# Performance work log

Measured on AMD Instinct MI355X. Metric: run time of the kernel, lower is better.

The kernel has to match this reference:

```python
import jax, jax.numpy as jnp
import numpy as np

K = 50          # NEC paper uses p=50 neighbors
DELTA = 1e-3    # kernel smoothing constant


def setup_inputs() -> dict:
    key = jax.random.key(0)
    ks = jax.random.split(key, 8)
    B, D_IN, D, A, C = 512, 2, 128, 3, 200000
    s = lambda fan_in: 1.0 / np.sqrt(fan_in)
    return {
        "x": jax.random.normal(ks[0], (B, D_IN), jnp.float32),
        "W1": jax.random.normal(ks[1], (D_IN, D), jnp.float32) * s(D_IN),
        "b1": jnp.zeros((D,), jnp.float32),
        "W2": jax.random.normal(ks[2], (D, D), jnp.float32) * s(D),
        "b2": jnp.zeros((D,), jnp.float32),
        "W3": jax.random.normal(ks[3], (D, D), jnp.float32) * s(D),
        "b3": jnp.zeros((D,), jnp.float32),
        "W4": jax.random.normal(ks[4], (D, D), jnp.float32) * s(D),
        "b4": jnp.zeros((D,), jnp.float32),
        "keys": jax.random.normal(ks[5], (A, C, D), jnp.float32),
        "mem_values": jax.random.normal(ks[6], (A, C), jnp.float32),
    }


def _encode(x, W1, b1, W2, b2, W3, b3, W4, b4):
    h = jax.nn.relu(x @ W1 + b1)
    h = jax.nn.relu(h @ W2 + b2)
    h = jax.nn.relu(h @ W3 + b3)
    return h @ W4 + b4  # [B, D]


def _dnd_lookup(h, keys, mem_values):
    # h: [B, D]; keys: [A, C, D]; mem_values: [A, C]
    q2 = jnp.sum(h * h, axis=-1)                       # [B]
    k2 = jnp.sum(keys * keys, axis=-1)                 # [A, C]
    cross = jnp.einsum("bd,acd->bac", h, keys)         # [B, A, C]
    d2 = jnp.maximum(q2[:, None, None] + k2[None] - 2.0 * cross, 0.0)
    neg_d, idx = jax.lax.top_k(-d2, K)                  # [B, A, K]
    d_top = -neg_d
    w = 1.0 / (d_top + DELTA)                           # NEC kernel
    w = w / jnp.sum(w, axis=-1, keepdims=True)
    a_idx = jnp.arange(keys.shape[0])[None, :, None]    # [1, A, 1]
    v_top = mem_values[a_idx, idx]                      # gather -> [B, A, K]
    values = jnp.sum(w * v_top, axis=-1)                # [B, A]
    return values


def reference(x, W1, b1, W2, b2, W3, b3, W4, b4, keys, mem_values):
    h = _encode(x, W1, b1, W2, b2, W3, b3, W4, b4)
    values = _dnd_lookup(h, keys, mem_values)
    actions = jnp.argmax(values, axis=-1)
    return values, actions
```

## Files before the change

kernel.cpp:

```cpp
#include <hip/hip_runtime.h>
#include <hip/hip_bf16.h>
#include <math.h>

#define B_    512
#define DIM   128
#define A_    3
#define C_    200000
#define K_    50
#define DELTA 1e-3

typedef __attribute__((ext_vector_type(8))) short bf16x8;
typedef __attribute__((ext_vector_type(4))) float f32x4;

#define NBIN_A 128
#define CAP_A  1024
#define ROWCH  12500

#define NSEG3  128
#define TPS3   25
#define NT3    3125

#define AOFF_H64   0u
#define AOFF_H32   524288u
#define AOFF_HBF   786432u
#define AOFF_Q2    917504u
#define AOFF_V64   1718272u
#define AOFF_BINS  8022016u
#define NEED_A     (8022016ull + 307200000ull)

#define NBIN_B 192
#define CAP_B  768
#define BM_B   64
#define BN_B   128
#define TPC_B  16
#define CHUNK_B (TPC_B*BN_B)
#define NCH_B  ((C_ + CHUNK_B - 1)/CHUNK_B)

#define BOFF_H32   0u
#define BOFF_H64   262144u
#define BOFF_Q2    786432u
#define BOFF_K2    788480u
#define BOFF_HIST  3188480u
#define BOFF_TAU   4368128u
#define BOFF_CNT   4374272u
#define BOFF_V64   4380416u
#define BOFF_CAND  4392704u

static __device__ inline unsigned short f2bf(float x) {
    union { float f; unsigned u; } c; c.f = x;
    unsigned r = (c.u + 0x7FFFu + ((c.u >> 16) & 1u)) >> 16;
    return (unsigned short)r;
}
static __device__ inline unsigned pkbf(float a, float b) {
    __hip_bfloat162 t = __float22bfloat162_rn(make_float2(a, b));
    union { __hip_bfloat162 h; unsigned u; } cv; cv.h = t; return cv.u;
}

__global__ __launch_bounds__(128) void mlp_kernel(
    const float* __restrict__ x,
    const float* __restrict__ W1, const float* __restrict__ b1,
    const float* __restrict__ W2, const float* __restrict__ b2,
    const float* __restrict__ W3, const float* __restrict__ b3,
    const float* __restrict__ W4, const float* __restrict__ b4,
    float* __restrict__ h32, unsigned short* __restrict__ hbf,
    double* __restrict__ h64, float* __restrict__ q2)
{
    int b = blockIdx.x, t = threadIdx.x;
    __shared__ double s0[DIM], s1[DIM];
    double x0 = (double)x[b*2+0], x1 = (double)x[b*2+1];
    double h = x0*(double)W1[t] + x1*(double)W1[DIM+t] + (double)b1[t];
    s0[t] = h > 0.0 ? h : 0.0;
    __syncthreads();
    double acc = (double)b2[t];
    for (int k = 0; k < DIM; k++) acc += s0[k]*(double)W2[k*DIM+t];
    s1[t] = acc > 0.0 ? acc : 0.0;
    __syncthreads();
    acc = (double)b3[t];
    for (int k = 0; k < DIM; k++) acc += s1[k]*(double)W3[k*DIM+t];
    s0[t] = acc > 0.0 ? acc : 0.0;
    __syncthreads();
    acc = (double)b4[t];
    for (int k = 0; k < DIM; k++) acc += s0[k]*(double)W4[k*DIM+t];
    h64[b*DIM+t] = acc;
    float hf = (float)acc;
    h32[b*DIM+t] = hf;
    hbf[b*DIM+t] = f2bf(hf);
    s1[t] = acc*acc;
    __syncthreads();
    for (int s = 64; s > 0; s >>= 1) { if (t < s) s1[t] += s1[t+s]; __syncthreads(); }
    if (t == 0) q2[b] = (float)s1[0];
}

static __device__ inline void load4(float4 lv[4], const float* __restrict__ ka,
                                    int nrow, int hh) {
    const float4* gp = (const float4*)(ka + (size_t)nrow*DIM) + hh*4;
    #pragma unroll
    for (int qq = 0; qq < 4; qq++) lv[qq] = gp[qq];
}
static __device__ inline void conv_store(const float4 lv[4], char* sBn,
                                         float* k2n, int r, int hh) {
    float ss = 0.f;
    int4 pk0, pk1;
    {
        float4 v0 = lv[0], v1 = lv[1];
        ss += v0.x*v0.x + v0.y*v0.y + v0.z*v0.z + v0.w*v0.w
            + v1.x*v1.x + v1.y*v1.y + v1.z*v1.z + v1.w*v1.w;
        pk0.x = (int)pkbf(v0.x, v0.y); pk0.y = (int)pkbf(v0.z, v0.w);
        pk0.z = (int)pkbf(v1.x, v1.y); pk0.w = (int)pkbf(v1.z, v1.w);
    }
    {
        float4 v0 = lv[2], v1 = lv[3];
        ss += v0.x*v0.x + v0.y*v0.y + v0.z*v0.z + v0.w*v0.w
            + v1.x*v1.x + v1.y*v1.y + v1.z*v1.z + v1.w*v1.w;
        pk1.x = (int)pkbf(v0.x, v0.y); pk1.y = (int)pkbf(v0.z, v0.w);
        pk1.z = (int)pkbf(v1.x, v1.y); pk1.w = (int)pkbf(v1.z, v1.w);
    }
    char* base = sBn + r*256;
    *(int4*)(base + (((hh*2    ) ^ (r & 7)) << 4)) = pk0;
    *(int4*)(base + (((hh*2 + 1) ^ (r & 7)) << 4)) = pk1;
    ss += __shfl_xor(ss, 1, 64);
    ss += __shfl_xor(ss, 2, 64);
    ss += __shfl_xor(ss, 4, 64);
    if (hh == 0) k2n[r] = ss;
}

__global__ __launch_bounds__(512, 2) void gemm3_kernel(
    const float* __restrict__ keys, const unsigned short* __restrict__ hbf,
    const float* __restrict__ q2, unsigned char* __restrict__ bins)
{
    const int seg = blockIdx.x, my = blockIdx.y, a = blockIdx.z;
    const int b0 = my*128;
    const int tid = threadIdx.x;
    const int lane = tid & 63, w = tid >> 6;
    const int lm = lane & 15, kh = lane >> 4;
    const int wn = w & 1, wm = w >> 1;

    const int tbeg = seg*TPS3;
    int tcnt = NT3 - tbeg;
    if (tcnt <= 0) return;
    if (tcnt > TPS3) tcnt = TPS3;

    __shared__ __align__(16) short sA[16384];
    __shared__ __align__(16) short sB[2][8192];
    __shared__ float q2s[128];
    __shared__ float k2s[2][64];

    {
        int r4 = tid >> 2, h4 = tid & 3;
        const int4* gp = (const int4*)hbf + (size_t)(b0 + r4)*16 + h4*4;
        #pragma unroll
        for (int qq = 0; qq < 4; qq++) {
            int cc = h4*4 + qq;
            *(int4*)((char*)sA + r4*256 + ((cc ^ (r4 & 7)) << 4)) = gp[qq];
        }
        if (tid < 128) q2s[tid] = q2[b0 + tid];
    }

    const int r = tid >> 3, hh = tid & 7;
    const float* ka = keys + (size_t)a*C_*DIM;

    float4 lv[4];
    load4(lv, ka, tbeg*64 + r, hh);
    conv_store(lv, (char*)&sB[0][0], k2s[0], r, hh);
    __syncthreads();

    int cur = 0;
    for (int t = 0; t < tcnt; t++) {
        const int n0 = (tbeg + t)*64;
        const bool more = (t + 1 < tcnt);

        if (more) load4(lv, ka, n0 + 64 + r, hh);

        f32x4 acc[2][2];
        #pragma unroll
        for (int i = 0; i < 2; i++)
            #pragma unroll
            for (int j = 0; j < 2; j++) acc[i][j] = (f32x4){0.f, 0.f, 0.f, 0.f};

        const char* sBc = (const char*)&sB[cur][0];
        #pragma unroll
        for (int kst = 0; kst < 4; kst++) {
            bf16x8 af[2], bfv[2];
            #pragma unroll
            for (int i = 0; i < 2; i++) {
                int nr = wn*32 + i*16 + lm;
                af[i] = *(const bf16x8*)(sBc + nr*256 + ((((kst<<2) + kh) ^ (nr & 7)) << 4));
            }
            #pragma unroll
            for (int j = 0; j < 2; j++) {
                int br = wm*32 + j*16 + lm;
                bfv[j] = *(const bf16x8*)((const char*)sA + br*256 + ((((kst<<2) + kh) ^ (br & 7)) << 4));
            }
            #pragma unroll
            for (int i = 0; i < 2; i++)
                #pragma unroll
                for (int j = 0; j < 2; j++)
                    acc[i][j] = __builtin_amdgcn_mfma_f32_16x16x32_bf16(af[i], bfv[j], acc[i][j], 0, 0, 0);
        }

        unsigned char* bp = bins + ((size_t)(a*B_ + b0))*C_ + n0;
        #pragma unroll
        for (int i = 0; i < 2; i++) {
            int nl = wn*32 + i*16 + kh*4;
            float4 kq = *(const float4*)&k2s[cur][nl];
            #pragma unroll
            for (int j = 0; j < 2; j++) {
                int bcol = wm*32 + j*16 + lm;
                float q2v = q2s[bcol];
                unsigned pk = 0;
                #pragma unroll
                for (int rg = 0; rg < 4; rg++) {
                    float kv = (rg == 0) ? kq.x : (rg == 1) ? kq.y : (rg == 2) ? kq.z : kq.w;
                    float d2v = (q2v + kv) - 2.0f*acc[i][j][rg];
                    float dc = fminf(fmaxf(d2v, 16.0f), 4095.0f);
                    unsigned bin = (__float_as_uint(dc) >> 19) - 2096u;
                    pk |= bin << (8*rg);
                }
                *(unsigned*)(bp + (size_t)bcol*C_ + nl) = pk;
            }
        }

        if (more) conv_store(lv, (char*)&sB[cur ^ 1][0], k2s[cur ^ 1], r, hh);
        __syncthreads();
        cur ^= 1;
    }
}

__global__ __launch_bounds__(256) void finish_kernel(
    const unsigned char* __restrict__ bins, const float* __restrict__ keys,
    const double* __restrict__ h64, const float* __restrict__ mem_values,
    float* __restrict__ out_values, double* __restrict__ val64)
{
    const int q = blockIdx.x;
    const int a = q >> 9, b = q & 511;
    const int p = b*A_ + a;
    const int tid = threadIdx.x;

    __shared__ unsigned hist_s[NBIN_A*8];
    __shared__ unsigned hc[NBIN_A];
    __shared__ double hd[DIM];
    __shared__ int    cidx[CAP_A];
    __shared__ double d2s[CAP_A];
    __shared__ float  vs[CAP_A];
    __shared__ double redv[4];
    __shared__ int    redi4[4];
    __shared__ double acc_w, acc_wv;
    __shared__ unsigned cnt_s;
    __shared__ int thr_s;

    for (int i = tid; i < NBIN_A*8; i += 256) hist_s[i] = 0;
    for (int i = tid; i < DIM; i += 256) hd[i] = h64[(size_t)b*DIM + i];
    if (tid == 0) { cnt_s = 0; acc_w = 0.0; acc_wv = 0.0; }
    __syncthreads();

    const uint4* row = (const uint4*)(bins + (size_t)q*C_);
    const int rep = tid & 7;
    for (int ch = tid; ch < ROWCH; ch += 256) {
        uint4 v = row[ch];
        unsigned d[4] = {v.x, v.y, v.z, v.w};
        #pragma unroll
        for (int e = 0; e < 4; e++) {
            unsigned x = d[e];
            atomicAdd(&hist_s[((x      ) & 127u)*8 + rep], 1u);
            atomicAdd(&hist_s[((x >>  8) & 127u)*8 + rep], 1u);
            atomicAdd(&hist_s[((x >> 16) & 127u)*8 + rep], 1u);
            atomicAdd(&hist_s[((x >> 24) & 127u)*8 + rep], 1u);
        }
    }
    __syncthreads();
    if (tid < NBIN_A) {
        unsigned s = 0;
        #pragma unroll
        for (int r2 = 0; r2 < 8; r2++) s += hist_s[tid*8 + r2];
        hc[tid] = s;
    }
    __syncthreads();
    if (tid == 0) {
        unsigned cum = 0; int jsel = NBIN_A-1;
        for (int j = 0; j < NBIN_A; j++) { cum += hc[j]; if (cum >= K_) { jsel = j; break; } }
        unsigned c1 = cum + (jsel+1 < NBIN_A ? hc[jsel+1] : 0u);
        unsigned c2 = c1  + (jsel+2 < NBIN_A ? hc[jsel+2] : 0u);
        int jt = (c2 <= 768u) ? jsel+2 : jsel+1;
        if (jt > NBIN_A-1) jt = NBIN_A-1;
        thr_s = jt + 1;
    }
    __syncthreads();
    const unsigned thr  = (unsigned)thr_s;
    const unsigned addv = (128u - thr) * 0x01010101u;
    for (int ch = tid; ch < ROWCH; ch += 256) {
        uint4 v = row[ch];
        unsigned d[4] = {v.x, v.y, v.z, v.w};
        #pragma unroll
        for (int e = 0; e < 4; e++) {
            unsigned m = (d[e] + addv) & 0x80808080u;
            if (m != 0x80808080u) {
                #pragma unroll
                for (int by = 0; by < 4; by++) {
                    if (!((m >> (8*by + 7)) & 1u)) {
                        unsigned pos = atomicAdd(&cnt_s, 1u);
                        if (pos < CAP_A) cidx[pos] = ch*16 + e*4 + by;
                    }
                }
            }
        }
    }
    __syncthreads();
    int n = (int)cnt_s; if (n > CAP_A) n = CAP_A;

    for (int i = tid; i < n; i += 256) {
        int c = cidx[i];
        const float4* kr = (const float4*)(keys + ((size_t)a*C_ + c)*DIM);
        double s0 = 0.0, s1 = 0.0;
        #pragma unroll 4
        for (int kq = 0; kq < 32; kq++) {
            float4 kv = kr[kq];
            double d0 = hd[4*kq+0] - (double)kv.x;
            double d1 = hd[4*kq+1] - (double)kv.y;
            double d2 = hd[4*kq+2] - (double)kv.z;
            double d3 = hd[4*kq+3] - (double)kv.w;
            s0 += d0*d0 + d1*d1; s1 += d2*d2 + d3*d3;
        }
        d2s[i] = s0 + s1;
        vs[i]  = mem_values[(size_t)a*C_ + c];
    }
    __syncthreads();

    int kk = n < K_ ? n : K_;
    for (int t = 0; t < kk; t++) {
        double best = 1e300; int bi = -1;
        for (int i = tid; i < n; i += 256)
            if (d2s[i] < best) { best = d2s[i]; bi = i; }
        #pragma unroll
        for (int off = 32; off > 0; off >>= 1) {
            double ov = __shfl_xor(best, off, 64);
            int    oi = __shfl_xor(bi,   off, 64);
            if (ov < best) { best = ov; bi = oi; }
        }
        int wv = tid >> 6;
        if ((tid & 63) == 0) { redv[wv] = best; redi4[wv] = bi; }
        __syncthreads();
        if (tid == 0) {
            double bv = redv[0]; int wi = redi4[0];
            if (redv[1] < bv) { bv = redv[1]; wi = redi4[1]; }
            if (redv[2] < bv) { bv = redv[2]; wi = redi4[2]; }
            if (redv[3] < bv) { bv = redv[3]; wi = redi4[3]; }
            double d = d2s[wi]; if (d < 0.0) d = 0.0;
            double wgt = 1.0 / (d + DELTA);
            acc_w += wgt; acc_wv += wgt * (double)vs[wi];
            d2s[wi] = 2e300;
        }
        __syncthreads();
    }
    if (tid == 0) {
        double v = acc_wv / acc_w;
        out_values[p] = (float)v;
        val64[p] = v;
    }
}

__global__ __launch_bounds__(256) void k2_kernel(const float* __restrict__ keys,
                                                 float* __restrict__ k2)
{
    int r = blockIdx.x*4 + (threadIdx.x >> 6);
    int lane = threadIdx.x & 63;
    float2 v = ((const float2*)keys)[(size_t)r*64 + lane];
    float s = v.x*v.x + v.y*v.y;
    #pragma unroll
    for (int off = 32; off > 0; off >>= 1) s += __shfl_down(s, off, 64);
    if (lane == 0) k2[r] = s;
}

template<int MODE>
__global__ __launch_bounds__(256) void pass_kernel(
    const float* __restrict__ keys, const float* __restrict__ h32,
    const float* __restrict__ q2,   const float* __restrict__ k2,
    unsigned* __restrict__ hist,    const float* __restrict__ tau,
    unsigned* __restrict__ cnt,     int* __restrict__ cand)
{
    const int bt = blockIdx.x;
    const int ch = blockIdx.y;
    const int a  = blockIdx.z;
    const int b0 = bt*BM_B;
    const int tid = threadIdx.x;
    const int tx = tid & 31, ty = tid >> 5;

    __shared__ float4 hs4[BM_B*33];
    __shared__ float4 ks4[BN_B*33];
    __shared__ float  q2s[BM_B];
    __shared__ float  taus[BM_B];
    __shared__ unsigned hist_s[MODE == 0 ? BM_B*NBIN_B : 1];

    #pragma unroll
    for (int q = 0; q < BM_B*32/256; q++) {
        int flat = q*256 + tid; int row = flat >> 5, kq = flat & 31;
        hs4[row*33 + kq] = ((const float4*)h32)[(size_t)(b0+row)*32 + kq];
    }
    if (tid < BM_B) {
        q2s[tid] = q2[b0+tid];
        if (MODE == 1) taus[tid] = tau[(b0+tid)*A_ + a];
    }
    if (MODE == 0) for (int i = tid; i < BM_B*NBIN_B; i += 256) hist_s[i] = 0;
    const float* __restrict__ k2g = k2 + (size_t)a*C_;

    for (int t = 0; t < TPC_B; t++) {
        int n0 = ch*CHUNK_B + t*BN_B;
        if (n0 >= C_) break;
        __syncthreads();
        #pragma unroll
        for (int q = 0; q < 16; q++) {
            int flat = q*256 + tid; int row = flat >> 5, kq = flat & 31;
            int nr = n0 + row; if (nr >= C_) nr = C_-1;
            ks4[row*33 + kq] = ((const float4*)keys)[((size_t)a*C_ + nr)*32 + kq];
        }
        __syncthreads();

        float acc[8][4];
        #pragma unroll
        for (int i = 0; i < 8; i++)
            #pragma unroll
            for (int j = 0; j < 4; j++) acc[i][j] = 0.0f;

        for (int kq = 0; kq < 32; kq++) {
            float4 hv[8], kv[4];
            #pragma unroll
            for (int i = 0; i < 8; i++) hv[i] = hs4[(ty*8+i)*33 + kq];
            #pragma unroll
            for (int j = 0; j < 4; j++) kv[j] = ks4[(j*32+tx)*33 + kq];
            #pragma unroll
            for (int i = 0; i < 8; i++)
                #pragma unroll
                for (int j = 0; j < 4; j++)
                    acc[i][j] += hv[i].x*kv[j].x + hv[i].y*kv[j].y
                               + hv[i].z*kv[j].z + hv[i].w*kv[j].w;
        }

        #pragma unroll
        for (int i = 0; i < 8; i++) {
            int bl = ty*8 + i;
            float q2b = q2s[bl];
            #pragma unroll
            for (int j = 0; j < 4; j++) {
                int n = n0 + j*32 + tx;
                if (n < C_) {
                    float d2f = fmaxf(q2b + k2g[n] - 2.0f*acc[i][j], 0.0f);
                    if (MODE == 0) {
                        int bin = (int)(__float_as_uint(d2f + 1.0f) >> 19) - 2032;
                        bin = bin < 0 ? 0 : (bin > NBIN_B-1 ? NBIN_B-1 : bin);
                        atomicAdd(&hist_s[bl*NBIN_B + bin], 1u);
                    } else {
                        if (d2f < taus[bl]) {
                            int p = (b0+bl)*A_ + a;
                            unsigned pos = atomicAdd(&cnt[p], 1u);
                            if (pos < CAP_B) cand[(size_t)p*CAP_B + pos] = n;
                        }
                    }
                }
            }
        }
    }
    if (MODE == 0) {
        __syncthreads();
        for (int i = tid; i < BM_B*NBIN_B; i += 256) {
            unsigned v = hist_s[i];
            if (v) {
                int bl = i / NBIN_B, bin = i % NBIN_B;
                atomicAdd(&hist[(size_t)((b0+bl)*A_ + a)*NBIN_B + bin], v);
            }
        }
    }
}

__global__ __launch_bounds__(256) void tauB_kernel(const unsigned* __restrict__ hist,
                                                   float* __restrict__ tau)
{
    int p = blockIdx.x*256 + threadIdx.x;
    if (p >= B_*A_) return;
    const unsigned* hp = hist + (size_t)p*NBIN_B;
    unsigned cum = 0; int jsel = NBIN_B-1;
    for (int j = 0; j < NBIN_B; j++) { cum += hp[j]; if (cum >= K_) { jsel = j; break; } }
    tau[p] = __uint_as_float((unsigned)(2034 + jsel) << 19) - 1.0f;
}

__global__ __launch_bounds__(256) void select_kernel(
    const float* __restrict__ keys, const double* __restrict__ h64,
    const float* __restrict__ mem_values,
    const unsigned* __restrict__ cnt, const int* __restrict__ cand,
    float* __restrict__ out_values, double* __restrict__ val64, int cap)
{
    int p = blockIdx.x; int b = p / A_, a = p % A_;
    int tid = threadIdx.x;
    __shared__ double hd[DIM];
    __shared__ double d2s[CAP_A];
    __shared__ float  vs[CAP_A];
    __shared__ double redv[4];
    __shared__ int    redi4[4];
    __shared__ double acc_w, acc_wv;

    for (int i = tid; i < DIM; i += 256) hd[i] = h64[(size_t)b*DIM + i];
    if (tid == 0) { acc_w = 0.0; acc_wv = 0.0; }
    __syncthreads();

    int n = (int)cnt[p]; if (n > cap) n = cap;
    for (int i = tid; i < n; i += 256) {
        int c = cand[(size_t)p*cap + i];
        const float4* kr = (const float4*)(keys + ((size_t)a*C_ + c)*DIM);
        double s0 = 0.0, s1 = 0.0;
        #pragma unroll 4
        for (int kq = 0; kq < 32; kq++) {
            float4 kv = kr[kq];
            double d0 = hd[4*kq+0] - (double)kv.x;
            double d1 = hd[4*kq+1] - (double)kv.y;
            double d2 = hd[4*kq+2] - (double)kv.z;
            double d3 = hd[4*kq+3] - (double)kv.w;
            s0 += d0*d0 + d1*d1; s1 += d2*d2 + d3*d3;
        }
        d2s[i] = s0 + s1;
        vs[i]  = mem_values[(size_t)a*C_ + c];
    }
    __syncthreads();

    int kk = n < K_ ? n : K_;
    for (int t = 0; t < kk; t++) {
        double best = 1e300; int bi = -1;
        for (int i = tid; i < n; i += 256)
            if (d2s[i] < best) { best = d2s[i]; bi = i; }
        #pragma unroll
        for (int off = 32; off > 0; off >>= 1) {
            double ov = __shfl_xor(best, off, 64);
            int    oi = __shfl_xor(bi,   off, 64);
            if (ov < best) { best = ov; bi = oi; }
        }
        int wv = tid >> 6;
        if ((tid & 63) == 0) { redv[wv] = best; redi4[wv] = bi; }
        __syncthreads();
        if (tid == 0) {
            double bv = redv[0]; int wi = redi4[0];
            if (redv[1] < bv) { bv = redv[1]; wi = redi4[1]; }
            if (redv[2] < bv) { bv = redv[2]; wi = redi4[2]; }
            if (redv[3] < bv) { bv = redv[3]; wi = redi4[3]; }
            double d = d2s[wi]; if (d < 0.0) d = 0.0;
            double wgt = 1.0 / (d + DELTA);
            acc_w += wgt; acc_wv += wgt * (double)vs[wi];
            d2s[wi] = 2e300;
        }
        __syncthreads();
    }
    if (tid == 0) {
        double v = acc_wv / acc_w;
        out_values[p] = (float)v;
        val64[p] = v;
    }
}

__global__ void argmax_kernel(const double* __restrict__ val64, float* __restrict__ out)
{
    int b = blockIdx.x*blockDim.x + threadIdx.x;
    if (b >= B_) return;
    double v0 = val64[b*A_+0], v1 = val64[b*A_+1], v2 = val64[b*A_+2];
    int bi = 0; double bv = v0;
    if (v1 > bv) { bv = v1; bi = 1; }
    if (v2 > bv) { bv = v2; bi = 2; }
    out[B_*A_ + b] = (float)bi;
}

extern "C" void kernel_launch(void* const* d_in, const int* in_sizes, int n_in,
                              void* d_out, int out_size, void* d_ws, size_t ws_size,
                              hipStream_t stream)
{
    const float* x    = (const float*)d_in[0];
    const float* W1   = (const float*)d_in[1];
    const float* b1   = (const float*)d_in[2];
    const float* W2   = (const float*)d_in[3];
    const float* b2   = (const float*)d_in[4];
    const float* W3   = (const float*)d_in[5];
    const float* b3   = (const float*)d_in[6];
    const float* W4   = (const float*)d_in[7];
    const float* b4   = (const float*)d_in[8];
    const float* keys = (const float*)d_in[9];
    const float* memv = (const float*)d_in[10];

    char* ws = (char*)d_ws;

    if (ws_size >= NEED_A) {
        double*         h64  = (double*)        (ws + AOFF_H64);
        float*          h32  = (float*)         (ws + AOFF_H32);
        unsigned short* hbf  = (unsigned short*)(ws + AOFF_HBF);
        float*          q2   = (float*)         (ws + AOFF_Q2);
        double*         v64  = (double*)        (ws + AOFF_V64);
        unsigned char*  bins = (unsigned char*) (ws + AOFF_BINS);

        mlp_kernel<<<B_, 128, 0, stream>>>(x, W1, b1, W2, b2, W3, b3, W4, b4, h32, hbf, h64, q2);
        gemm3_kernel<<<dim3(NSEG3, 4, A_), 512, 0, stream>>>(keys, hbf, q2, bins);
        finish_kernel<<<B_*A_, 256, 0, stream>>>(bins, keys, h64, memv, (float*)d_out, v64);
        argmax_kernel<<<2, 256, 0, stream>>>(v64, (float*)d_out);
    } else {
        float*          h32  = (float*)         (ws + BOFF_H32);
        double*         h64  = (double*)        (ws + BOFF_H64);
        float*          q2   = (float*)         (ws + BOFF_Q2);
        float*          k2   = (float*)         (ws + BOFF_K2);
        unsigned*       hist = (unsigned*)      (ws + BOFF_HIST);
        float*          tau  = (float*)         (ws + BOFF_TAU);
        unsigned*       cnt  = (unsigned*)      (ws + BOFF_CNT);
        double*         v64  = (double*)        (ws + BOFF_V64);
        int*            cand = (int*)           (ws + BOFF_CAND);
        unsigned short* hbf  = (unsigned short*)(ws + BOFF_CAND);

        hipMemsetAsync(ws + BOFF_HIST, 0, (BOFF_CNT + B_*A_*4) - BOFF_HIST, stream);

        mlp_kernel<<<B_, 128, 0, stream>>>(x, W1, b1, W2, b2, W3, b3, W4, b4, h32, hbf, h64, q2);
        k2_kernel<<<(A_*C_)/4, 256, 0, stream>>>(keys, k2);
        pass_kernel<0><<<dim3(B_/BM_B, NCH_B, A_), 256, 0, stream>>>(keys, h32, q2, k2, hist, nullptr, nullptr, nullptr);
        tauB_kernel<<<(B_*A_ + 255)/256, 256, 0, stream>>>(hist, tau);
        pass_kernel<1><<<dim3(B_/BM_B, NCH_B, A_), 256, 0, stream>>>(keys, h32, q2, k2, nullptr, tau, cnt, cand);
        select_kernel<<<B_*A_, 256, 0, stream>>>(keys, h64, memv, cnt, cand, (float*)d_out, v64, CAP_B);
        argmax_kernel<<<2, 256, 0, stream>>>(v64, (float*)d_out);
    }
}
```

Before: 960.1 us.

## Shrink GEMM query tile to 64 rows, defer bin stores, widen histogram replicas

The distance GEMM now processes 64 query rows per block instead of 128, with twice as many blocks and a launch bound of 6 blocks per SM. This lowers per-block LDS and register use so more blocks can be resident at once. Each tile's packed bin bytes are written one iteration later, so the global store overlaps the next tile's MFMA work. The finish kernel's shared histogram now keeps 16 replicas per bin, indexed by wave and lane, to reduce atomic contention. The cost is that each block re-reads the keys tile twice as often, which adds global traffic.

```diff
diff --git a/kernel.cpp b/kernel.cpp
--- a/kernel.cpp
+++ b/kernel.cpp
@@ -124,12 +124,12 @@
     if (hh == 0) k2n[r] = ss;
 }
 
-__global__ __launch_bounds__(512, 2) void gemm3_kernel(
+__global__ __launch_bounds__(512, 6) void gemm3_kernel(
     const float* __restrict__ keys, const unsigned short* __restrict__ hbf,
     const float* __restrict__ q2, unsigned char* __restrict__ bins)
 {
     const int seg = blockIdx.x, my = blockIdx.y, a = blockIdx.z;
-    const int b0 = my*128;
+    const int b0 = my*64;
     const int tid = threadIdx.x;
     const int lane = tid & 63, w = tid >> 6;
     const int lm = lane & 15, kh = lane >> 4;
@@ -140,20 +140,20 @@
     if (tcnt <= 0) return;
     if (tcnt > TPS3) tcnt = TPS3;
 
-    __shared__ __align__(16) short sA[16384];
+    __shared__ __align__(16) short sA[8192];
     __shared__ __align__(16) short sB[2][8192];
-    __shared__ float q2s[128];
+    __shared__ float q2s[64];
     __shared__ float k2s[2][64];
 
     {
-        int r4 = tid >> 2, h4 = tid & 3;
-        const int4* gp = (const int4*)hbf + (size_t)(b0 + r4)*16 + h4*4;
-        #pragma unroll
-        for (int qq = 0; qq < 4; qq++) {
-            int cc = h4*4 + qq;
-            *(int4*)((char*)sA + r4*256 + ((cc ^ (r4 & 7)) << 4)) = gp[qq];
-        }
-        if (tid < 128) q2s[tid] = q2[b0 + tid];
+        #pragma unroll
+        for (int u = 0; u < 2; u++) {
+            int idx = tid*2 + u;
+            int rr = idx >> 4, cc = idx & 15;
+            const int4 gv = ((const int4*)hbf)[(size_t)(b0 + rr)*16 + cc];
+            *(int4*)((char*)sA + rr*256 + ((cc ^ (rr & 7)) << 4)) = gv;
+        }
+        if (tid < 64) q2s[tid] = q2[b0 + tid];
     }
 
     const int r = tid >> 3, hh = tid & 7;
@@ -163,6 +163,14 @@
     load4(lv, ka, tbeg*64 + r, hh);
     conv_store(lv, (char*)&sB[0][0], k2s[0], r, hh);
     __syncthreads();
+
+    unsigned char* bp_base = bins + ((size_t)(a*B_ + b0))*C_;
+    const int bcol = wm*16 + lm;
+    const size_t soff0 = (size_t)bcol*C_ + (wn*32 + 0*16 + kh*4);
+    const size_t soff1 = (size_t)bcol*C_ + (wn*32 + 1*16 + kh*4);
+
+    unsigned pk_prev0 = 0, pk_prev1 = 0;
+    int n0_prev = 0;
 
     int cur = 0;
     for (int t = 0; t < tcnt; t++) {
@@ -170,60 +178,59 @@
         const bool more = (t + 1 < tcnt);
 
         if (more) load4(lv, ka, n0 + 64 + r, hh);
-
-        f32x4 acc[2][2];
-        #pragma unroll
-        for (int i = 0; i < 2; i++)
-            #pragma unroll
-            for (int j = 0; j < 2; j++) acc[i][j] = (f32x4){0.f, 0.f, 0.f, 0.f};
+        if (t > 0) {
+            *(unsigned*)(bp_base + n0_prev + soff0) = pk_prev0;
+            *(unsigned*)(bp_base + n0_prev + soff1) = pk_prev1;
+        }
+
+        f32x4 acc[2];
+        acc[0] = (f32x4){0.f, 0.f, 0.f, 0.f};
+        acc[1] = (f32x4){0.f, 0.f, 0.f, 0.f};
 
         const char* sBc = (const char*)&sB[cur][0];
         #pragma unroll
         for (int kst = 0; kst < 4; kst++) {
-            bf16x8 af[2], bfv[2];
+            bf16x8 af[2], bfv;
             #pragma unroll
             for (int i = 0; i < 2; i++) {
                 int nr = wn*32 + i*16 + lm;
                 af[i] = *(const bf16x8*)(sBc + nr*256 + ((((kst<<2) + kh) ^ (nr & 7)) << 4));
             }
-            #pragma unroll
-            for (int j = 0; j < 2; j++) {
-                int br = wm*32 + j*16 + lm;
-                bfv[j] = *(const bf16x8*)((const char*)sA + br*256 + ((((kst<<2) + kh) ^ (br & 7)) << 4));
+            {
+                int br = wm*16 + lm;
+                bfv = *(const bf16x8*)((const char*)sA + br*256 + ((((kst<<2) + kh) ^ (br & 7)) << 4));
             }
             #pragma unroll
             for (int i = 0; i < 2; i++)
-                #pragma unroll
-                for (int j = 0; j < 2; j++)
-                    acc[i][j] = __builtin_amdgcn_mfma_f32_16x16x32_bf16(af[i], bfv[j], acc[i][j], 0, 0, 0);
-        }
-
-        unsigned char* bp = bins + ((size_t)(a*B_ + b0))*C_ + n0;
-        #pragma unroll
-        for (int i = 0; i < 2; i++) {
-            int nl = wn*32 + i*16 + kh*4;
-            float4 kq = *(const float4*)&k2s[cur][nl];
-            #pragma unroll
-            for (int j = 0; j < 2; j++) {
-                int bcol = wm*32 + j*16 + lm;
-                float q2v = q2s[bcol];
+                acc[i] = __builtin_amdgcn_mfma_f32_16x16x32_bf16(af[i], bfv, acc[i], 0, 0, 0);
+        }
+
+        {
+            const float q2v = q2s[bcol];
+            #pragma unroll
+            for (int i = 0; i < 2; i++) {
+                int nl = wn*32 + i*16 + kh*4;
+                float4 kq = *(const float4*)&k2s[cur][nl];
                 unsigned pk = 0;
                 #pragma unroll
                 for (int rg = 0; rg < 4; rg++) {
                     float kv = (rg == 0) ? kq.x : (rg == 1) ? kq.y : (rg == 2) ? kq.z : kq.w;
-                    float d2v = (q2v + kv) - 2.0f*acc[i][j][rg];
+                    float d2v = (q2v + kv) - 2.0f*acc[i][rg];
                     float dc = fminf(fmaxf(d2v, 16.0f), 4095.0f);
                     unsigned bin = (__float_as_uint(dc) >> 19) - 2096u;
                     pk |= bin << (8*rg);
                 }
-                *(unsigned*)(bp + (size_t)bcol*C_ + nl) = pk;
+                if (i == 0) pk_prev0 = pk; else pk_prev1 = pk;
             }
+            n0_prev = n0;
         }
 
         if (more) conv_store(lv, (char*)&sB[cur ^ 1][0], k2s[cur ^ 1], r, hh);
         __syncthreads();
         cur ^= 1;
     }
+    *(unsigned*)(bp_base + n0_prev + soff0) = pk_prev0;
+    *(unsigned*)(bp_base + n0_prev + soff1) = pk_prev1;
 }
 
 __global__ __launch_bounds__(256) void finish_kernel(
@@ -236,7 +243,7 @@
     const int p = b*A_ + a;
     const int tid = threadIdx.x;
 
-    __shared__ unsigned hist_s[NBIN_A*8];
+    __shared__ unsigned hist_s[NBIN_A*16];
     __shared__ unsigned hc[NBIN_A];
     __shared__ double hd[DIM];
     __shared__ int    cidx[CAP_A];
@@ -248,30 +255,30 @@
     __shared__ unsigned cnt_s;
     __shared__ int thr_s;
 
-    for (int i = tid; i < NBIN_A*8; i += 256) hist_s[i] = 0;
+    for (int i = tid; i < NBIN_A*16; i += 256) hist_s[i] = 0;
     for (int i = tid; i < DIM; i += 256) hd[i] = h64[(size_t)b*DIM + i];
     if (tid == 0) { cnt_s = 0; acc_w = 0.0; acc_wv = 0.0; }
     __syncthreads();
 
     const uint4* row = (const uint4*)(bins + (size_t)q*C_);
-    const int rep = tid & 7;
+    const int rep = ((tid >> 6) << 2) | (tid & 3);
     for (int ch = tid; ch < ROWCH; ch += 256) {
         uint4 v = row[ch];
         unsigned d[4] = {v.x, v.y, v.z, v.w};
         #pragma unroll
         for (int e = 0; e < 4; e++) {
             unsigned x = d[e];
-            atomicAdd(&hist_s[((x      ) & 127u)*8 + rep], 1u);
-            atomicAdd(&hist_s[((x >>  8) & 127u)*8 + rep], 1u);
-            atomicAdd(&hist_s[((x >> 16) & 127u)*8 + rep], 1u);
-            atomicAdd(&hist_s[((x >> 24) & 127u)*8 + rep], 1u);
+            atomicAdd(&hist_s[((x      ) & 127u)*16 + rep], 1u);
+            atomicAdd(&hist_s[((x >>  8) & 127u)*16 + rep], 1u);
+            atomicAdd(&hist_s[((x >> 16) & 127u)*16 + rep], 1u);
+            atomicAdd(&hist_s[((x >> 24) & 127u)*16 + rep], 1u);
         }
     }
     __syncthreads();
     if (tid < NBIN_A) {
         unsigned s = 0;
         #pragma unroll
-        for (int r2 = 0; r2 < 8; r2++) s += hist_s[tid*8 + r2];
+        for (int r2 = 0; r2 < 16; r2++) s += hist_s[tid*16 + r2];
         hc[tid] = s;
     }
     __syncthreads();
@@ -590,7 +597,7 @@
         unsigned char*  bins = (unsigned char*) (ws + AOFF_BINS);
 
         mlp_kernel<<<B_, 128, 0, stream>>>(x, W1, b1, W2, b2, W3, b3, W4, b4, h32, hbf, h64, q2);
-        gemm3_kernel<<<dim3(NSEG3, 4, A_), 512, 0, stream>>>(keys, hbf, q2, bins);
+        gemm3_kernel<<<dim3(NSEG3, 8, A_), 512, 0, stream>>>(keys, hbf, q2, bins);
         finish_kernel<<<B_*A_, 256, 0, stream>>>(bins, keys, h64, memv, (float*)d_out, v64);
         argmax_kernel<<<2, 256, 0, stream>>>(v64, (float*)d_out);
     } else {
```

After: 1.098 ms. +14.4%, slower.
